# Optimization experiments

Measured on AMD Instinct MI355X. Metric: run time of the kernel, lower is better.

The kernel has to match this reference:

```python
import jax, jax.numpy as jnp
import numpy as np

BIG = 1e30  # stand-in for +inf at DP boundaries (never selected by min)


def setup_inputs() -> dict:
    key = jax.random.key(0)
    kx, kp = jax.random.split(key)
    B, D, T = 32, 16, 1024        # batch, channels (d_patts), stream length
    P, L = 64, 32                 # n_patts, l_patts
    x = jax.random.normal(kx, (B, D, T), dtype=jnp.float32)
    patts = jax.random.normal(kp, (P, D, L), dtype=jnp.float32)
    rho = 0.5
    w = float(rho ** (1.0 / L))   # self.w = rho ** (1 / l_patts)
    return {"x": x, "patts": patts, "w": w}


def _dtw(x, patts, w):
    # Weighted streaming DTW: for each pattern p and each ending time j,
    # D[i, j] = cost[i, j] + min(D[i-1, j], w*D[i, j-1], w*D[i-1, j-1])
    # with D[i, 0] = cost[i, 0] + D[i-1, 0] (first time column cumsum) and
    # cost[i, j] = ||x[:, j] - patts[:, i]||^2 (squared euclidean over channels).
    B, D, T = x.shape
    P, _, L = patts.shape
    p2 = jnp.sum(patts * patts, axis=1)                       # (P, L)

    def cost_at(xj):                                          # xj: (B, D)
        x2 = jnp.sum(xj * xj, axis=1)                         # (B,)
        xp = jnp.einsum('bd,pdl->bpl', xj, patts)             # (B, P, L)
        return x2[:, None, None] + p2[None] - 2.0 * xp        # (B, P, L)

    # first time column
    col0 = jnp.cumsum(cost_at(x[:, :, 0]), axis=-1)           # (B, P, L)

    def step(prev, xj):
        cost = cost_at(xj)                                    # (B, P, L)
        prev_up = jnp.concatenate(
            [jnp.full_like(prev[..., :1], BIG), prev[..., :-1]], axis=-1)
        m = w * jnp.minimum(prev, prev_up)                    # (B, P, L)

        def inner(new_im1, cm):                               # scan along pattern axis
            c_i, m_i = cm
            new_i = c_i + jnp.minimum(new_im1, m_i)
            return new_i, new_i

        _, new = jax.lax.scan(
            inner, jnp.full((B, P), BIG, cost.dtype),
            (jnp.moveaxis(cost, -1, 0), jnp.moveaxis(m, -1, 0)))
        new_col = jnp.moveaxis(new, 0, -1)                    # (B, P, L)
        return new_col, new_col[..., -1]                      # emit full-pattern match cost

    xs = jnp.moveaxis(x[:, :, 1:], -1, 0)                     # (T-1, B, D)
    _, rest = jax.lax.scan(step, col0, xs)                    # (T-1, B, P)
    dtw = jnp.concatenate([col0[None, ..., -1], rest], axis=0)  # (T, B, P)
    return jnp.moveaxis(dtw, 0, -1)                           # (B, P, T)


def reference(x, patts, w):
    return jnp.sqrt(_dtw(x, patts, w))
```

## Files before the change

### kernel.cpp

```cpp
#include <hip/hip_runtime.h>
#include <math.h>

#define B_ 32
#define D_ 16
#define T_ 1024
#define P_ 64
#define L_ 32
#define KB 524288.0f

typedef short short8 __attribute__((ext_vector_type(8)));
typedef float f32x4 __attribute__((ext_vector_type(4)));
typedef unsigned short ushort_t;

template<int CTRL, int ROW_MASK, bool BC>
__device__ __forceinline__ float dpp_mov(float old_, float src) {
  int o = __builtin_bit_cast(int, old_);
  int s = __builtin_bit_cast(int, src);
  int r = __builtin_amdgcn_update_dpp(o, s, CTRL, ROW_MASK, 0xf, BC);
  return __builtin_bit_cast(float, r);
}

__device__ __forceinline__ float scan_sum32(float v) {
  v += dpp_mov<0x111, 0xf, true>(0.f, v);
  v += dpp_mov<0x112, 0xf, true>(0.f, v);
  v += dpp_mov<0x114, 0xf, true>(0.f, v);
  v += dpp_mov<0x118, 0xf, true>(0.f, v);
  v += dpp_mov<0x142, 0xa, false>(0.f, v);
  return v;
}

__device__ __forceinline__ float scan_max32(float v) {
  asm("s_nop 1\n\t"
      "v_max_f32_dpp %0, %0, %0 row_shr:1 row_mask:0xf bank_mask:0xf\n\t"
      "s_nop 1\n\t"
      "v_max_f32_dpp %0, %0, %0 row_shr:2 row_mask:0xf bank_mask:0xf\n\t"
      "s_nop 1\n\t"
      "v_max_f32_dpp %0, %0, %0 row_shr:4 row_mask:0xf bank_mask:0xf\n\t"
      "s_nop 1\n\t"
      "v_max_f32_dpp %0, %0, %0 row_shr:8 row_mask:0xf bank_mask:0xf\n\t"
      "s_nop 1\n\t"
      "v_max_f32_dpp %0, %0, %0 row_bcast:15 row_mask:0xa bank_mask:0xf"
      : "+v"(v));
  return v;
}

__device__ __forceinline__ ushort_t f2bf(float f) {
  unsigned u = __builtin_bit_cast(unsigned, f);
  return (ushort_t)((u + 0x7FFFu + ((u >> 16) & 1u)) >> 16);
}
__device__ __forceinline__ float bf2f(ushort_t h) {
  unsigned u = ((unsigned)h) << 16;
  return __builtin_bit_cast(float, u);
}

__global__ __launch_bounds__(256) void prep_fused(
    const float* __restrict__ x, const float* __restrict__ patts,
    ushort_t* __restrict__ xA, ushort_t* __restrict__ pB) {
  const int bid = blockIdx.x;
  if (bid < 128) {
    int gid = bid * 256 + threadIdx.x;
    int b = gid >> 10, t = gid & 1023;
    float x2 = 0.f;
    ushort_t o[32];
#pragma unroll
    for (int d = 0; d < 16; ++d) {
      float v = x[((b * 16 + d) << 10) + t];
      x2 = fmaf(v, v, x2);
      o[d] = f2bf(v);
    }
    o[16] = 0x3F80; o[17] = 0x3F80;
    ushort_t hi = f2bf(x2);
    o[18] = hi;
    o[19] = f2bf(x2 - bf2f(hi));
#pragma unroll
    for (int d = 20; d < 32; ++d) o[d] = 0;
    uint4* dst = (uint4*)(xA + (size_t)gid * 32);
#pragma unroll
    for (int q = 0; q < 4; ++q) {
      const ushort_t* s = o + q * 8;
      uint4 u;
      u.x = (unsigned)s[0] | ((unsigned)s[1] << 16);
      u.y = (unsigned)s[2] | ((unsigned)s[3] << 16);
      u.z = (unsigned)s[4] | ((unsigned)s[5] << 16);
      u.w = (unsigned)s[6] | ((unsigned)s[7] << 16);
      dst[q] = u;
    }
  } else {
    __shared__ float Ls[4][16 * 33];
    __shared__ float Lh[4][64];
    __shared__ float LP2[4][32];
    const int sub = threadIdx.x >> 6;
    const int l = threadIdx.x & 63;
    const int p = (bid - 128) * 4 + sub;
    const int half = l >> 5;
    const int m = l & 31;

    float p2acc = 0.f;
#pragma unroll
    for (int dd = 0; dd < 16; dd += 2) {
      int d = dd + half;
      float v = patts[((p * 16 + d) << 5) + m];
      p2acc = fmaf(v, v, p2acc);
      Ls[sub][d * 33 + m] = scan_sum32(v);
    }
    Lh[sub][l] = p2acc;
    __syncthreads();
    {
      float tot = Lh[sub][m] + Lh[sub][32 + m];
      float pref = scan_sum32(tot);
      if (half == 0) LP2[sub][m] = pref;
    }
    __syncthreads();

    const int n = l & 15, q = l >> 4;
#pragma unroll
    for (int iblk = 0; iblk < 2; ++iblk) {
      const int i = iblk * 16 + n;
      ushort_t o[8];
      if (q < 2) {
#pragma unroll
        for (int e = 0; e < 8; ++e)
          o[e] = f2bf(-2.f * Ls[sub][(q * 8 + e) * 33 + i]);
      } else if (q == 2) {
        float P2 = LP2[sub][i];
        ushort_t hi = f2bf(P2);
        o[0] = hi; o[1] = f2bf(P2 - bf2f(hi));
        o[2] = f2bf((float)(i + 1)); o[3] = o[2];
        o[4] = o[5] = o[6] = o[7] = 0;
      } else {
#pragma unroll
        for (int e = 0; e < 8; ++e) o[e] = 0;
      }
      uint4 u;
      u.x = (unsigned)o[0] | ((unsigned)o[1] << 16);
      u.y = (unsigned)o[2] | ((unsigned)o[3] << 16);
      u.z = (unsigned)o[4] | ((unsigned)o[5] << 16);
      u.w = (unsigned)o[6] | ((unsigned)o[7] << 16);
      ((uint4*)pB)[(p * 2 + iblk) * 64 + l] = u;
    }
  }
}

__global__ __launch_bounds__(64, 4) void dtw_kernel(
    const ushort_t* __restrict__ xA,
    const ushort_t* __restrict__ pBg,
    const float* __restrict__ wp,
    float* __restrict__ out)
{
  __shared__ float lds[2640];

  const int l   = threadIdx.x;
  const int li  = l & 31;
  const int g   = l >> 5;
  const int q4  = l >> 4;
  const unsigned bx = blockIdx.x;
  const int ch   = bx & 3u;
  const unsigned rest = bx >> 2;
  const int b  = rest >> 5;
  const int pA = (rest & 31) << 1;
  const float w = wp[0];
  const float nw = -w;
  const bool l0c = (li == 0), l31 = (li == 31);

  const int S0    = (ch == 0) ? 0 : (ch == 1) ? 6 : (ch == 2) ? 20 : 34;
  const int nT    = (ch == 0) ? 22 : 30;
  const int warmT = (ch == 0) ? 0 : 16;

  const short8* pBs = (const short8*)pBg;
  short8 B00 = pBs[((pA    ) * 2 + 0) * 64 + l];
  short8 B01 = pBs[((pA    ) * 2 + 1) * 64 + l];
  short8 B10 = pBs[((pA + 1) * 2 + 0) * 64 + l];
  short8 B11 = pBs[((pA + 1) * 2 + 1) * 64 + l];

  const short8* xAs = (const short8*)xA + ((size_t)b << 12);

  short8 Aa;
  auto loadA = [&](int t) {
    Aa = xAs[((((S0 + t) << 4) + (l & 15)) << 2) + q4];
  };

  float* ldsW = lds + 20 + (l & 15) * 20 + q4 * 4;
  const float* ldsR  = lds + 20 + g * 660 + li * 20;
  const float* ldsRx = ldsR - 20;

  if (l < 20) {
    lds[l] = KB; lds[660 + l] = KB; lds[1320 + l] = KB; lds[1980 + l] = KB;
  }
  __syncthreads();

  const f32x4 zk = {KB, KB, KB, KB};

  auto fill = [&](int bufsel) {
    float* wb = ldsW + bufsel * 1320;
    f32x4 d0 = __builtin_amdgcn_mfma_f32_16x16x32_bf16(Aa, B00, zk, 0, 0, 0);
    f32x4 d1 = __builtin_amdgcn_mfma_f32_16x16x32_bf16(Aa, B01, zk, 0, 0, 0);
    f32x4 d2 = __builtin_amdgcn_mfma_f32_16x16x32_bf16(Aa, B10, zk, 0, 0, 0);
    f32x4 d3 = __builtin_amdgcn_mfma_f32_16x16x32_bf16(Aa, B11, zk, 0, 0, 0);
    *(f32x4*)(wb + 0)   = d0;
    *(f32x4*)(wb + 320) = d1;
    *(f32x4*)(wb + 660) = d2;
    *(f32x4*)(wb + 980) = d3;
  };

  float* orow = out + (((size_t)(b * P_ + pA + g)) << 10) + (S0 << 4);
  float dcur = 0.f;

  auto DP = [&](int bufsel, bool first, bool store, float* op) {
    const float* rb = ldsR  + bufsel * 1320;
    const float* rx = ldsRx + bufsel * 1320;
    f32x4 s0 = *(const f32x4*)(rb + 0);
    f32x4 x0 = *(const f32x4*)(rx + 0);
    f32x4 s1 = *(const f32x4*)(rb + 4);
    f32x4 x1 = *(const f32x4*)(rx + 4);
    f32x4 s2 = *(const f32x4*)(rb + 8);
    f32x4 x2 = *(const f32x4*)(rx + 8);
    f32x4 s3 = *(const f32x4*)(rb + 12);
    f32x4 x3 = *(const f32x4*)(rx + 12);
    float4 r0, r1, r2, r3;
#pragma unroll
    for (int k4 = 0; k4 < 4; ++k4) {
      f32x4 Sq = (k4 == 0) ? s0 : (k4 == 1) ? s1 : (k4 == 2) ? s2 : s3;
      f32x4 Xq = (k4 == 0) ? x0 : (k4 == 1) ? x1 : (k4 == 2) ? x2 : x3;
      float4 rv;
#pragma unroll
      for (int e = 0; e < 4; ++e) {
        float Zo = Sq[e];
        float Zx = Xq[e];
        float a = fmaf(nw, dcur, Zx);
        float c = fmaf(nw, dcur, Zo);
        float u;
        asm("s_nop 1\n\t"
            "v_max_f32_dpp %0, %1, %2 wave_shr:1 row_mask:0xf bank_mask:0xf"
            : "=&v"(u) : "v"(c), "v"(a));
        u = l0c ? a : u;
        float Mx = scan_max32(u);
        float val = Zo - Mx;
        if (first && k4 == 0 && e == 0)
          val = Zo - KB;
        dcur = val;
        if (e == 0) rv.x = val; else if (e == 1) rv.y = val;
        else if (e == 2) rv.z = val; else rv.w = val;
      }
      if (k4 == 0) r0 = rv; else if (k4 == 1) r1 = rv;
      else if (k4 == 2) r2 = rv; else r3 = rv;
    }
    if (store) {
      if (l31) {
        float4 s;
        s.x = __builtin_amdgcn_sqrtf(r0.x); s.y = __builtin_amdgcn_sqrtf(r0.y);
        s.z = __builtin_amdgcn_sqrtf(r0.z); s.w = __builtin_amdgcn_sqrtf(r0.w);
        *(float4*)(op + 0) = s;
        s.x = __builtin_amdgcn_sqrtf(r1.x); s.y = __builtin_amdgcn_sqrtf(r1.y);
        s.z = __builtin_amdgcn_sqrtf(r1.z); s.w = __builtin_amdgcn_sqrtf(r1.w);
        *(float4*)(op + 4) = s;
        s.x = __builtin_amdgcn_sqrtf(r2.x); s.y = __builtin_amdgcn_sqrtf(r2.y);
        s.z = __builtin_amdgcn_sqrtf(r2.z); s.w = __builtin_amdgcn_sqrtf(r2.w);
        *(float4*)(op + 8) = s;
        s.x = __builtin_amdgcn_sqrtf(r3.x); s.y = __builtin_amdgcn_sqrtf(r3.y);
        s.z = __builtin_amdgcn_sqrtf(r3.z); s.w = __builtin_amdgcn_sqrtf(r3.w);
        *(float4*)(op + 12) = s;
      }
    }
  };

  loadA(0);
  fill(0);
  loadA(1);
  for (int t = 0; t < nT; ++t) {
    if (t + 1 < nT) fill((t & 1) ^ 1);
    if (t + 2 < nT) loadA(t + 2);
    DP(t & 1, t == 0, t >= warmT, orow + (t << 4));
  }
}

extern "C" void kernel_launch(void* const* d_in, const int* in_sizes, int n_in,
                              void* d_out, int out_size, void* d_ws, size_t ws_size,
                              hipStream_t stream) {
  const float* x     = (const float*)d_in[0];
  const float* patts = (const float*)d_in[1];
  const float* w     = (const float*)d_in[2];
  float* out = (float*)d_out;

  ushort_t* xA = (ushort_t*)d_ws;
  ushort_t* pB = (ushort_t*)((char*)d_ws + (size_t)B_ * T_ * 32 * 2);

  prep_fused<<<144, 256, 0, stream>>>(x, patts, xA, pB);
  dtw_kernel<<<B_ * (P_ / 2) * 4, 64, 0, stream>>>(xA, pB, w, out);
}
```

Before: 124.3 us.

## Pack four DTW waves per block, single-buffer LDS, rebalance time chunks

Each block now runs four independent wavefronts, each handling two patterns with its own LDS region, in place of one wave per block. The LDS cost tile drops from double to single buffering: the DP reads its slice into registers before the next MFMA fill overwrites it. The four time chunks are made uniform (28 steps each, start every 12 tiles, 16-step warmup), which shortens the longest chunk's serial recurrence from 30 steps. This relies on in-order LDS access within a wave for the single buffer, and changes occupancy and scheduling granularity.

```diff
diff --git a/kernel.cpp b/kernel.cpp
--- a/kernel.cpp
+++ b/kernel.cpp
@@ -141,30 +141,33 @@
   }
 }
 
-__global__ __launch_bounds__(64, 4) void dtw_kernel(
+__global__ __launch_bounds__(256, 4) void dtw_kernel(
     const ushort_t* __restrict__ xA,
     const ushort_t* __restrict__ pBg,
     const float* __restrict__ wp,
     float* __restrict__ out)
 {
-  __shared__ float lds[2640];
-
-  const int l   = threadIdx.x;
+  __shared__ float lds[4 * 1320];
+
+  const int tid = threadIdx.x;
+  const int l   = tid & 63;
+  const int wid = tid >> 6;
   const int li  = l & 31;
   const int g   = l >> 5;
   const int q4  = l >> 4;
   const unsigned bx = blockIdx.x;
   const int ch   = bx & 3u;
   const unsigned rest = bx >> 2;
-  const int b  = rest >> 5;
-  const int pA = (rest & 31) << 1;
+  const int b     = rest >> 3;
+  const int pbase = (rest & 7) << 3;
+  const int pA  = pbase + (wid << 1);
   const float w = wp[0];
   const float nw = -w;
   const bool l0c = (li == 0), l31 = (li == 31);
 
-  const int S0    = (ch == 0) ? 0 : (ch == 1) ? 6 : (ch == 2) ? 20 : 34;
-  const int nT    = (ch == 0) ? 22 : 30;
-  const int warmT = (ch == 0) ? 0 : 16;
+  const int S0    = ch * 12;
+  const int nT    = 28;
+  const int warmT = ch ? 16 : 0;
 
   const short8* pBs = (const short8*)pBg;
   short8 B00 = pBs[((pA    ) * 2 + 0) * 64 + l];
@@ -179,43 +182,51 @@
     Aa = xAs[((((S0 + t) << 4) + (l & 15)) << 2) + q4];
   };
 
-  float* ldsW = lds + 20 + (l & 15) * 20 + q4 * 4;
-  const float* ldsR  = lds + 20 + g * 660 + li * 20;
+  float* base = lds + wid * 1320;
+  float* ldsW = base + 20 + (l & 15) * 20 + q4 * 4;
+  const float* ldsR  = base + 20 + g * 660 + li * 20;
   const float* ldsRx = ldsR - 20;
 
-  if (l < 20) {
-    lds[l] = KB; lds[660 + l] = KB; lds[1320 + l] = KB; lds[1980 + l] = KB;
-  }
+  if (l < 20) { base[l] = KB; base[660 + l] = KB; }
   __syncthreads();
 
   const f32x4 zk = {KB, KB, KB, KB};
 
-  auto fill = [&](int bufsel) {
-    float* wb = ldsW + bufsel * 1320;
+  auto fill = [&]() {
     f32x4 d0 = __builtin_amdgcn_mfma_f32_16x16x32_bf16(Aa, B00, zk, 0, 0, 0);
     f32x4 d1 = __builtin_amdgcn_mfma_f32_16x16x32_bf16(Aa, B01, zk, 0, 0, 0);
     f32x4 d2 = __builtin_amdgcn_mfma_f32_16x16x32_bf16(Aa, B10, zk, 0, 0, 0);
     f32x4 d3 = __builtin_amdgcn_mfma_f32_16x16x32_bf16(Aa, B11, zk, 0, 0, 0);
-    *(f32x4*)(wb + 0)   = d0;
-    *(f32x4*)(wb + 320) = d1;
-    *(f32x4*)(wb + 660) = d2;
-    *(f32x4*)(wb + 980) = d3;
+    *(f32x4*)(ldsW + 0)   = d0;
+    *(f32x4*)(ldsW + 320) = d1;
+    *(f32x4*)(ldsW + 660) = d2;
+    *(f32x4*)(ldsW + 980) = d3;
   };
 
   float* orow = out + (((size_t)(b * P_ + pA + g)) << 10) + (S0 << 4);
   float dcur = 0.f;
 
-  auto DP = [&](int bufsel, bool first, bool store, float* op) {
-    const float* rb = ldsR  + bufsel * 1320;
-    const float* rx = ldsRx + bufsel * 1320;
-    f32x4 s0 = *(const f32x4*)(rb + 0);
-    f32x4 x0 = *(const f32x4*)(rx + 0);
-    f32x4 s1 = *(const f32x4*)(rb + 4);
-    f32x4 x1 = *(const f32x4*)(rx + 4);
-    f32x4 s2 = *(const f32x4*)(rb + 8);
-    f32x4 x2 = *(const f32x4*)(rx + 8);
-    f32x4 s3 = *(const f32x4*)(rb + 12);
-    f32x4 x3 = *(const f32x4*)(rx + 12);
+  loadA(0);
+  fill();
+  loadA(1);
+
+  for (int t = 0; t < nT; ++t) {
+    f32x4 s0 = *(const f32x4*)(ldsR + 0);
+    f32x4 x0 = *(const f32x4*)(ldsRx + 0);
+    f32x4 s1 = *(const f32x4*)(ldsR + 4);
+    f32x4 x1 = *(const f32x4*)(ldsRx + 4);
+    f32x4 s2 = *(const f32x4*)(ldsR + 8);
+    f32x4 x2 = *(const f32x4*)(ldsRx + 8);
+    f32x4 s3 = *(const f32x4*)(ldsR + 12);
+    f32x4 x3 = *(const f32x4*)(ldsRx + 12);
+
+    if (t + 1 < nT) fill();
+    if (t + 2 < nT) loadA(t + 2);
+
+    const bool first = (t == 0);
+    const bool store = (t >= warmT);
+    float* op = orow + (t << 4);
+
     float4 r0, r1, r2, r3;
 #pragma unroll
     for (int k4 = 0; k4 < 4; ++k4) {
@@ -261,15 +272,6 @@
         *(float4*)(op + 12) = s;
       }
     }
-  };
-
-  loadA(0);
-  fill(0);
-  loadA(1);
-  for (int t = 0; t < nT; ++t) {
-    if (t + 1 < nT) fill((t & 1) ^ 1);
-    if (t + 2 < nT) loadA(t + 2);
-    DP(t & 1, t == 0, t >= warmT, orow + (t << 4));
   }
 }
 
@@ -285,5 +287,5 @@
   ushort_t* pB = (ushort_t*)((char*)d_ws + (size_t)B_ * T_ * 32 * 2);
 
   prep_fused<<<144, 256, 0, stream>>>(x, patts, xA, pB);
-  dtw_kernel<<<B_ * (P_ / 2) * 4, 64, 0, stream>>>(xA, pB, w, out);
-}
+  dtw_kernel<<<B_ * (P_ / 8) * 4, 256, 0, stream>>>(xA, pB, w, out);
+}
```

Result: faster. 109.8 us (-11.7%).
